# Performance work log

Hardware: AMD Instinct MI355X
Metric: run time of the kernel (lower is better)

Reference implementation:

```python
import jax, jax.numpy as jnp
import numpy as np

# static multi-scale feature pyramid (strides 8/16/32/64 of ~800px input)
SPATIAL = ((100, 100), (50, 50), (25, 25), (13, 13))
L = 4          # num_levels
NH = 8         # num_heads
NP = 4         # num_points
E = 256        # embed_dim
HD = E // NH   # head dim = 32
NLAYERS = 6
FFN_DIM = 1024
T = sum(h * w for h, w in SPATIAL)  # 13294 total tokens
B = 2


def _layer_norm(x, g, b, eps=1e-5):
    m = jnp.mean(x, -1, keepdims=True)
    v = jnp.mean((x - m) ** 2, -1, keepdims=True)
    return (x - m) * jax.lax.rsqrt(v + eps) * g + b


def _get_reference_points(valid_ratios):
    # valid_ratios: [B, L, 2] (wx, hy)
    refs = []
    for lvl, (H_, W_) in enumerate(SPATIAL):
        ry, rx = jnp.meshgrid(
            jnp.linspace(0.5, H_ - 0.5, H_, dtype=jnp.float32),
            jnp.linspace(0.5, W_ - 0.5, W_, dtype=jnp.float32),
            indexing='ij')
        ry = ry.reshape(-1)[None] / (valid_ratios[:, None, lvl, 1] * H_)
        rx = rx.reshape(-1)[None] / (valid_ratios[:, None, lvl, 0] * W_)
        refs.append(jnp.stack([rx, ry], -1))            # [B, H*W, 2]
    ref = jnp.concatenate(refs, 1)                       # [B, T, 2]
    return ref[:, :, None] * valid_ratios[:, None]       # [B, T, L, 2]


def _msda(value, loc, attn_w):
    # value: [B, T, NH, HD]; loc: [B, Q, NH, L, NP, 2] in [0,1]; attn_w: [B, Q, NH, L, NP]
    Bv, Tv, H, D = value.shape
    Q = loc.shape[1]
    out = jnp.zeros((Bv, Q, H, D), value.dtype)
    start = 0
    for lvl, (h, w) in enumerate(SPATIAL):
        v = value[:, start:start + h * w].transpose(0, 2, 1, 3)  # [B, NH, hw, D]
        start += h * w
        g = loc[:, :, :, lvl]                                    # [B, Q, NH, NP, 2]
        # grid_sample semantics, align_corners=False: pixel = g*size - 0.5
        x = g[..., 0] * w - 0.5
        y = g[..., 1] * h - 0.5
        x0 = jnp.floor(x).astype(jnp.int32)
        y0 = jnp.floor(y).astype(jnp.int32)
        wx = x - x0
        wy = y - y0

        def corner(ix, iy, cw):
            valid = (ix >= 0) & (ix < w) & (iy >= 0) & (iy < h)
            idx = jnp.clip(iy, 0, h - 1) * w + jnp.clip(ix, 0, w - 1)  # [B,Q,NH,NP]
            idx_t = idx.transpose(0, 2, 1, 3).reshape(Bv, H, Q * NP)
            gath = jnp.take_along_axis(v, idx_t[..., None], axis=2)    # [B,NH,QP,D]
            gath = gath.reshape(Bv, H, Q, NP, D)
            m = valid.transpose(0, 2, 1, 3)[..., None].astype(value.dtype)
            cw_t = cw.transpose(0, 2, 1, 3)[..., None]
            return gath * m * cw_t

        samp = (corner(x0, y0, (1 - wx) * (1 - wy))
                + corner(x0 + 1, y0, wx * (1 - wy))
                + corner(x0, y0 + 1, (1 - wx) * wy)
                + corner(x0 + 1, y0 + 1, wx * wy))  # [B,NH,Q,NP,D]
        out = out + jnp.einsum('bhqpd,bqhp->bqhd', samp, attn_w[:, :, :, lvl])
    return out.reshape(Bv, Q, H * D)


# offset normalizer (W, H) per level, as in Deformable-DETR
_OFF_NORM = jnp.array([[w, h] for (h, w) in SPATIAL], jnp.float32)  # [L, 2]


def _block(src, pos, ref, mask, p):
    (Wv, bv, Woff, boff, Wattn, battn, Wout, bout,
     n1g, n1b, n2g, n2b, W1, b1, W2, b2) = p
    x = _layer_norm(src, n1g, n1b)
    q = x + pos
    value = x @ Wv + bv
    value = jnp.where(mask[:, :, None], 0.0, value).reshape(B, T, NH, HD)
    off = (q @ Woff + boff).reshape(B, T, NH, L, NP, 2)
    attn = (q @ Wattn + battn).reshape(B, T, NH, L * NP)
    attn = jax.nn.softmax(attn, -1).reshape(B, T, NH, L, NP)
    loc = ref[:, :, None, :, None, :] + off / _OFF_NORM[None, None, None, :, None, :]
    attn_out = _msda(value, loc, attn) @ Wout + bout
    src = src + attn_out
    x = _layer_norm(src, n2g, n2b)
    ffn = jax.nn.relu(x @ W1 + b1) @ W2 + b2
    return src + ffn


def setup_inputs() -> dict:
    key = jax.random.key(0)
    ks = jax.random.split(key, 24)

    def rn(k, shape, scale=0.02):
        return jax.random.normal(k, shape, jnp.float32) * scale

    inp = {
        'src': jax.random.normal(ks[0], (B, T, E), jnp.float32),
        'pos': jax.random.normal(ks[1], (B, T, E), jnp.float32),
        'valid_ratios': jnp.ones((B, L, 2), jnp.float32),
        'spatial_shapes': jnp.array(SPATIAL, jnp.int32),
        'level_start_index': jnp.array(
            np.concatenate([[0], np.cumsum([h * w for h, w in SPATIAL])[:-1]]), jnp.int32),
        'mask': jnp.zeros((B, T), bool),
        # per-layer stacked parameters [NLAYERS, ...]
        'Wv': rn(ks[2], (NLAYERS, E, E)),
        'bv': jnp.zeros((NLAYERS, E), jnp.float32),
        'Woff': rn(ks[3], (NLAYERS, E, NH * L * NP * 2)),
        'boff': rn(ks[4], (NLAYERS, NH * L * NP * 2), 0.5),
        'Wattn': rn(ks[5], (NLAYERS, E, NH * L * NP)),
        'battn': jnp.zeros((NLAYERS, NH * L * NP), jnp.float32),
        'Wout': rn(ks[6], (NLAYERS, E, E)),
        'bout': jnp.zeros((NLAYERS, E), jnp.float32),
        'n1g': jnp.ones((NLAYERS, E), jnp.float32),
        'n1b': jnp.zeros((NLAYERS, E), jnp.float32),
        'n2g': jnp.ones((NLAYERS, E), jnp.float32),
        'n2b': jnp.zeros((NLAYERS, E), jnp.float32),
        'W1': rn(ks[7], (NLAYERS, E, FFN_DIM)),
        'b1': jnp.zeros((NLAYERS, FFN_DIM), jnp.float32),
        'W2': rn(ks[8], (NLAYERS, FFN_DIM, E)),
        'b2': jnp.zeros((NLAYERS, E), jnp.float32),
    }
    return inp


def reference(src, pos, valid_ratios, spatial_shapes, level_start_index, mask,
              Wv, bv, Woff, boff, Wattn, battn, Wout, bout,
              n1g, n1b, n2g, n2b, W1, b1, W2, b2):
    # spatial_shapes / level_start_index are encoded statically in SPATIAL (values match)
    ref = _get_reference_points(valid_ratios)  # [B, T, L, 2]
    x = src
    stacked = (Wv, bv, Woff, boff, Wattn, battn, Wout, bout,
               n1g, n1b, n2g, n2b, W1, b1, W2, b2)
    for i in range(NLAYERS):
        p = tuple(a[i] for a in stacked)
        x = _block(x, pos, ref, mask, p)
    return x
```

## Files before the change

### kernel.cpp

```cpp
#include <hip/hip_runtime.h>
#include <hip/hip_bf16.h>

#define NLAYERS 6
#define Bc 2
#define Tc 13294
#define Ec 256
#define NHc 8
#define FFNc 1024

#define EPI_BIAS 0
#define EPI_MASK 1
#define EPI_RES  2
#define EPI_RELU 3

typedef __attribute__((ext_vector_type(8))) short bf16x8;
typedef __attribute__((ext_vector_type(4))) float f32x4;

typedef __attribute__((address_space(3))) unsigned int u32_lds;
typedef __attribute__((address_space(1))) unsigned int u32_glb;

__device__ __forceinline__ void gld16(const void* g, void* l) {
    __builtin_amdgcn_global_load_lds((const u32_glb*)g, (u32_lds*)l, 16, 0, 0);
}

__device__ __forceinline__ short f2bf(float f) {
    union { float f; unsigned u; } v; v.f = f;
    unsigned r = v.u + 0x7FFFu + ((v.u >> 16) & 1u);
    return (short)(r >> 16);
}
__device__ __forceinline__ float bf2f(short s) {
    union { unsigned u; float f; } v; v.u = ((unsigned)(unsigned short)s) << 16;
    return v.f;
}
__device__ __forceinline__ float bf_lo(unsigned u) {
    union { unsigned u; float f; } v; v.u = u << 16; return v.f;
}
__device__ __forceinline__ float bf_hi(unsigned u) {
    union { unsigned u; float f; } v; v.u = u & 0xFFFF0000u; return v.f;
}

__global__ __launch_bounds__(256) void ln_kernel(
    const float* __restrict__ src, const float* __restrict__ pos,
    const float* __restrict__ g, const float* __restrict__ b,
    short* __restrict__ x, short* __restrict__ q, int rows)
{
    int wave = threadIdx.x >> 6;
    int lane = threadIdx.x & 63;
    int row = blockIdx.x * 4 + wave;
    if (row >= rows) return;
    const float* p = src + (size_t)row * Ec;
    float4 v = *(const float4*)(p + lane * 4);
    float s  = v.x + v.y + v.z + v.w;
    float sq = v.x*v.x + v.y*v.y + v.z*v.z + v.w*v.w;
    #pragma unroll
    for (int o = 32; o; o >>= 1) { s += __shfl_xor(s, o); sq += __shfl_xor(sq, o); }
    float mean = s * (1.f / Ec);
    float var  = sq * (1.f / Ec) - mean * mean;
    float inv  = rsqrtf(var + 1e-5f);
    float4 gg = *(const float4*)(g + lane * 4);
    float4 bb = *(const float4*)(b + lane * 4);
    float xo0 = (v.x - mean) * inv * gg.x + bb.x;
    float xo1 = (v.y - mean) * inv * gg.y + bb.y;
    float xo2 = (v.z - mean) * inv * gg.z + bb.z;
    float xo3 = (v.w - mean) * inv * gg.w + bb.w;
    short4 xs; xs.x = f2bf(xo0); xs.y = f2bf(xo1); xs.z = f2bf(xo2); xs.w = f2bf(xo3);
    *(short4*)(x + (size_t)row * Ec + lane * 4) = xs;
    if (q) {
        float4 pp = *(const float4*)(pos + (size_t)row * Ec + lane * 4);
        short4 qs;
        qs.x = f2bf(xo0 + pp.x); qs.y = f2bf(xo1 + pp.y);
        qs.z = f2bf(xo2 + pp.z); qs.w = f2bf(xo3 + pp.w);
        *(short4*)(q + (size_t)row * Ec + lane * 4) = qs;
    }
}

__global__ __launch_bounds__(256) void transpose_w(
    const float* __restrict__ W, short* __restrict__ Wt, int K, int N,
    int layerStride, int rowOff)
{
    __shared__ float tile[32][33];
    int l = blockIdx.z;
    const float* Wl = W + (size_t)l * K * N;
    short* Wtl = Wt + (size_t)l * layerStride;
    int n0 = blockIdx.x * 32, k0 = blockIdx.y * 32;
    int tx = threadIdx.x & 31, ty = threadIdx.x >> 5;
    #pragma unroll
    for (int i = 0; i < 32; i += 8)
        tile[ty + i][tx] = Wl[(size_t)(k0 + ty + i) * N + n0 + tx];
    __syncthreads();
    #pragma unroll
    for (int i = 0; i < 32; i += 8)
        Wtl[(size_t)(rowOff + n0 + ty + i) * K + k0 + tx] = f2bf(tile[tx][ty + i]);
}

template<int EPI, int OBF>
__global__ __launch_bounds__(256) void gemm_mfma(
    const short* __restrict__ A, const short* __restrict__ Bt,
    const float* __restrict__ bias, const float* __restrict__ bias2,
    const float* __restrict__ res, const unsigned char* __restrict__ mask,
    void* __restrict__ Cout, int M, int N, int K)
{
    __shared__ short As[2][128 * 32];
    __shared__ short Bs[2][64 * 32];
    const int tid = threadIdx.x;
    const int lane = tid & 63;
    const int wv = tid >> 6;
    const int row0 = blockIdx.x * 128;
    const int col0 = blockIdx.y * 64;
    const int mbase = (wv >> 1) * 64;
    const int nbase = (wv & 1) * 32;
    const int lr = lane & 15;
    const int kg = lane >> 4;

    f32x4 zf = {0.f, 0.f, 0.f, 0.f};
    f32x4 acc[4][2];
    #pragma unroll
    for (int i = 0; i < 4; ++i)
        #pragma unroll
        for (int j = 0; j < 2; ++j) acc[i][j] = zf;

    const int scol = (lane & 3) * 8;
    const int srowA = wv * 32 + (lane >> 2);
    const short* Ap = A + (size_t)(row0 + srowA) * K + scol;
    const int lA0 = srowA * 32 + scol;
    const int lA1 = lA0 + 16 * 32;
    const int srowB = wv * 16 + (lane >> 2);
    const short* Bp = Bt + (size_t)(col0 + srowB) * K + scol;
    const int lB = srowB * 32 + scol;

    #define STAGE(buf, k0) do { \
        gld16(Ap + (k0),                &As[buf][lA0]); \
        gld16(Ap + (size_t)16*K + (k0), &As[buf][lA1]); \
        gld16(Bp + (k0),                &Bs[buf][lB]); \
    } while (0)

    STAGE(0, 0);
    __syncthreads();
    int cur = 0;
    for (int k0 = 0; k0 < K; k0 += 32) {
        if (k0 + 32 < K) STAGE(cur ^ 1, k0 + 32);
        bf16x8 af[4], bfr[2];
        #pragma unroll
        for (int i = 0; i < 4; ++i)
            af[i]  = *(const bf16x8*)&As[cur][(mbase + i * 16 + lr) * 32 + kg * 8];
        #pragma unroll
        for (int j = 0; j < 2; ++j)
            bfr[j] = *(const bf16x8*)&Bs[cur][(nbase + j * 16 + lr) * 32 + kg * 8];
        #pragma unroll
        for (int mi = 0; mi < 4; ++mi)
            #pragma unroll
            for (int ni = 0; ni < 2; ++ni)
                acc[mi][ni] = __builtin_amdgcn_mfma_f32_16x16x32_bf16(
                    af[mi], bfr[ni], acc[mi][ni], 0, 0, 0);
        __syncthreads();
        cur ^= 1;
    }
    #undef STAGE

    float* Cf = (float*)Cout;
    short* Cb = (short*)Cout;
    #pragma unroll
    for (int ni = 0; ni < 2; ++ni) {
        int col = col0 + nbase + ni * 16 + lr;
        float bz = (bias2 && col >= 256) ? bias2[col - 256] : bias[col];
        #pragma unroll
        for (int mi = 0; mi < 4; ++mi) {
            int rb = row0 + mbase + mi * 16 + kg * 4;
            #pragma unroll
            for (int j = 0; j < 4; ++j) {
                int grow = rb + j;
                if (grow >= M) continue;
                float v = acc[mi][ni][j] + bz;
                if (EPI == EPI_MASK) { if (mask[grow]) v = 0.f; }
                if (EPI == EPI_RES)  v += res[(size_t)grow * N + col];
                if (EPI == EPI_RELU) v = v > 0.f ? v : 0.f;
                if (OBF) Cb[(size_t)grow * N + col] = f2bf(v);
                else     Cf[(size_t)grow * N + col] = v;
            }
        }
    }
}

__global__ __launch_bounds__(256) void msda_kernel(
    const short* __restrict__ value, const short* __restrict__ oa,
    const float* __restrict__ vr, short* __restrict__ out)
{
    __shared__ int pts[8 * 136];
    const int group = threadIdx.x >> 5;
    const int l32 = threadIdx.x & 31;
    const int gidx = blockIdx.x * 8 + group;
    const int h = gidx & 7;
    const int bq = gidx >> 3;
    const int b = (bq >= Tc) ? 1 : 0;
    const int qq = bq - b * Tc;

    if (l32 < 16) {
        const int p = l32;
        const int lvl = p >> 2;
        const int Wl[4] = {100, 50, 25, 13};
        const int St[4] = {0, 10000, 12500, 13125};
        float base_x, base_y;
        if (qq < 10000) {
            int qi = qq;
            base_x = (0.5f + (float)(qi % 100)) / (vr[(b*4+0)*2+0] * 100.f);
            base_y = (0.5f + (float)(qi / 100)) / (vr[(b*4+0)*2+1] * 100.f);
        } else if (qq < 12500) {
            int qi = qq - 10000;
            base_x = (0.5f + (float)(qi % 50)) / (vr[(b*4+1)*2+0] * 50.f);
            base_y = (0.5f + (float)(qi / 50)) / (vr[(b*4+1)*2+1] * 50.f);
        } else if (qq < 13125) {
            int qi = qq - 12500;
            base_x = (0.5f + (float)(qi % 25)) / (vr[(b*4+2)*2+0] * 25.f);
            base_y = (0.5f + (float)(qi / 25)) / (vr[(b*4+2)*2+1] * 25.f);
        } else {
            int qi = qq - 13125;
            base_x = (0.5f + (float)(qi % 13)) / (vr[(b*4+3)*2+0] * 13.f);
            base_y = (0.5f + (float)(qi / 13)) / (vr[(b*4+3)*2+1] * 13.f);
        }
        float logit = bf2f(oa[(size_t)bq * 384 + 256 + h * 16 + p]);
        float mx = logit;
        #pragma unroll
        for (int o = 8; o; o >>= 1) mx = fmaxf(mx, __shfl_xor(mx, o));
        float e = expf(logit - mx);
        float sum = e;
        #pragma unroll
        for (int o = 8; o; o >>= 1) sum += __shfl_xor(sum, o);
        float aw = e / sum;

        const int w = Wl[lvl], hh = Wl[lvl];
        const float refx = base_x * vr[(b*4+lvl)*2+0];
        const float refy = base_y * vr[(b*4+lvl)*2+1];
        const float ox = bf2f(oa[(size_t)bq * 384 + h * 32 + p * 2 + 0]);
        const float oy = bf2f(oa[(size_t)bq * 384 + h * 32 + p * 2 + 1]);
        float locx = refx + ox / (float)w;
        float locy = refy + oy / (float)hh;
        float xf = locx * (float)w - 0.5f;
        float yf = locy * (float)hh - 0.5f;
        float x0f = floorf(xf), y0f = floorf(yf);
        int x0 = (int)x0f, y0 = (int)y0f;
        float wx = xf - x0f, wy = yf - y0f;
        float w00 = (1.f - wx) * (1.f - wy) * aw;
        float w10 = wx * (1.f - wy) * aw;
        float w01 = (1.f - wx) * wy * aw;
        float w11 = wx * wy * aw;
        bool vx0 = (x0 >= 0) && (x0 < w);
        bool vx1 = (x0 + 1 >= 0) && (x0 + 1 < w);
        bool vy0 = (y0 >= 0) && (y0 < hh);
        bool vy1 = (y0 + 1 >= 0) && (y0 + 1 < hh);
        if (!(vx0 && vy0)) w00 = 0.f;
        if (!(vx1 && vy0)) w10 = 0.f;
        if (!(vx0 && vy1)) w01 = 0.f;
        if (!(vx1 && vy1)) w11 = 0.f;
        int cx0 = min(max(x0, 0), w - 1), cx1 = min(max(x0 + 1, 0), w - 1);
        int cy0 = min(max(y0, 0), hh - 1), cy1 = min(max(y0 + 1, 0), hh - 1);
        int rowbase = b * Tc + St[lvl];
        int slot = group * 136 + p * 8 + ((p >> 3) & 1) * 4;
        int4 wq4; wq4.x = __float_as_int(w00); wq4.y = __float_as_int(w10);
        wq4.z = __float_as_int(w01); wq4.w = __float_as_int(w11);
        int4 aq4;
        aq4.x = (rowbase + cy0 * w + cx0) * 512 + h * 64;
        aq4.y = (rowbase + cy0 * w + cx1) * 512 + h * 64;
        aq4.z = (rowbase + cy1 * w + cx0) * 512 + h * 64;
        aq4.w = (rowbase + cy1 * w + cx1) * 512 + h * 64;
        *(int4*)&pts[slot] = wq4;
        *(int4*)&pts[slot + 4] = aq4;
    }
    __syncthreads();

    const int d4 = (l32 & 15) * 4;
    const int ph = (l32 >> 4) * 8;
    const int xw = (l32 >> 4) * 4;
    const char* vbase = (const char*)value;
    float accL = 0.f, accH = 0.f;
    #pragma unroll
    for (int j = 0; j < 8; ++j) {
        int p = ph + j;
        int slot = group * 136 + p * 8 + xw;
        int4 wq = *(const int4*)&pts[slot];
        int4 aq = *(const int4*)&pts[slot + 4];
        unsigned u0 = *(const unsigned*)(vbase + (unsigned)(aq.x + d4));
        unsigned u1 = *(const unsigned*)(vbase + (unsigned)(aq.y + d4));
        unsigned u2 = *(const unsigned*)(vbase + (unsigned)(aq.z + d4));
        unsigned u3 = *(const unsigned*)(vbase + (unsigned)(aq.w + d4));
        float w00 = __int_as_float(wq.x), w10 = __int_as_float(wq.y);
        float w01 = __int_as_float(wq.z), w11 = __int_as_float(wq.w);
        accL = fmaf(w00, bf_lo(u0), accL); accH = fmaf(w00, bf_hi(u0), accH);
        accL = fmaf(w10, bf_lo(u1), accL); accH = fmaf(w10, bf_hi(u1), accH);
        accL = fmaf(w01, bf_lo(u2), accL); accH = fmaf(w01, bf_hi(u2), accH);
        accL = fmaf(w11, bf_lo(u3), accL); accH = fmaf(w11, bf_hi(u3), accH);
    }
    accL += __shfl_xor(accL, 16);
    accH += __shfl_xor(accH, 16);
    if (l32 < 16) {
        unsigned pk = ((unsigned)(unsigned short)f2bf(accL)) |
                      (((unsigned)(unsigned short)f2bf(accH)) << 16);
        *(unsigned*)((char*)out + (size_t)bq * 512 + h * 64 + d4) = pk;
    }
}

extern "C" void kernel_launch(void* const* d_in, const int* in_sizes, int n_in,
                              void* d_out, int out_size, void* d_ws, size_t ws_size,
                              hipStream_t stream) {
    const float* src  = (const float*)d_in[0];
    const float* pos  = (const float*)d_in[1];
    const float* vr   = (const float*)d_in[2];
    const unsigned char* mask = (const unsigned char*)d_in[5];
    const float* Wv    = (const float*)d_in[6];
    const float* bv    = (const float*)d_in[7];
    const float* Woff  = (const float*)d_in[8];
    const float* boff  = (const float*)d_in[9];
    const float* Wattn = (const float*)d_in[10];
    const float* battn = (const float*)d_in[11];
    const float* Wout  = (const float*)d_in[12];
    const float* bout  = (const float*)d_in[13];
    const float* n1g   = (const float*)d_in[14];
    const float* n1b   = (const float*)d_in[15];
    const float* n2g   = (const float*)d_in[16];
    const float* n2b   = (const float*)d_in[17];
    const float* W1    = (const float*)d_in[18];
    const float* b1    = (const float*)d_in[19];
    const float* W2    = (const float*)d_in[20];
    const float* b2    = (const float*)d_in[21];
    float* out = (float*)d_out;

    const size_t R = (size_t)Bc * Tc;

    short* xb    = (short*)d_ws;
    short* qb    = xb + R * 256;
    short* valb  = qb + R * 256;
    short* msdab = valb + R * 256;
    short* oab   = msdab + R * 256;
    short* ln2b  = xb;
    short* hb    = qb;
    float* srcb  = (float*)(oab + R * 384);
    short* wvT   = (short*)(srcb + R * 256);
    short* woaT  = wvT + 6 * 65536;
    short* woutT = woaT + 6 * 98304;
    short* w1T   = woutT + 6 * 65536;
    short* w2T   = w1T + 6 * 262144;

    transpose_w<<<dim3(8, 8, 6),  256, 0, stream>>>(Wv,    wvT,   256, 256,  65536, 0);
    transpose_w<<<dim3(8, 8, 6),  256, 0, stream>>>(Woff,  woaT,  256, 256,  98304, 0);
    transpose_w<<<dim3(4, 8, 6),  256, 0, stream>>>(Wattn, woaT,  256, 128,  98304, 256);
    transpose_w<<<dim3(8, 8, 6),  256, 0, stream>>>(Wout,  woutT, 256, 256,  65536, 0);
    transpose_w<<<dim3(32, 8, 6), 256, 0, stream>>>(W1,    w1T,   256, 1024, 262144, 0);
    transpose_w<<<dim3(8, 32, 6), 256, 0, stream>>>(W2,    w2T,   1024, 256, 262144, 0);

    const int lnBlocks = (int)((R + 3) / 4);
    const int MT = (int)((R + 127) / 128);

    for (int l = 0; l < NLAYERS; ++l) {
        const float* cur = (l == 0) ? src : srcb;
        ln_kernel<<<lnBlocks, 256, 0, stream>>>(cur, pos, n1g + l * Ec, n1b + l * Ec, xb, qb, (int)R);
        gemm_mfma<EPI_MASK, 1><<<dim3(MT, 4), 256, 0, stream>>>(
            xb, wvT + (size_t)l * 65536, bv + l * Ec, nullptr, nullptr, mask, valb, (int)R, 256, 256);
        gemm_mfma<EPI_BIAS, 1><<<dim3(MT, 6), 256, 0, stream>>>(
            qb, woaT + (size_t)l * 98304, boff + l * 256, battn + l * 128, nullptr, nullptr,
            oab, (int)R, 384, 256);
        msda_kernel<<<(int)R, 256, 0, stream>>>(valb, oab, vr, msdab);
        gemm_mfma<EPI_RES, 0><<<dim3(MT, 4), 256, 0, stream>>>(
            msdab, woutT + (size_t)l * 65536, bout + l * Ec, nullptr, cur, nullptr, srcb, (int)R, 256, 256);
        ln_kernel<<<lnBlocks, 256, 0, stream>>>(srcb, nullptr, n2g + l * Ec, n2b + l * Ec, ln2b, nullptr, (int)R);
        gemm_mfma<EPI_RELU, 1><<<dim3(MT, 16), 256, 0, stream>>>(
            ln2b, w1T + (size_t)l * 262144, b1 + l * FFNc, nullptr, nullptr, nullptr, hb, (int)R, 1024, 256);
        float* dst = (l == NLAYERS - 1) ? out : srcb;
        gemm_mfma<EPI_RES, 0><<<dim3(MT, 4), 256, 0, stream>>>(
            hb, w2T + (size_t)l * 262144, b2 + l * Ec, nullptr, srcb, nullptr, dst, (int)R, 256, 1024);
    }
}
```

Baseline: 1.250 ms.

## Fuse LayerNorm into full-row GEMM epilogues and enlarge FFN/offset GEMM tiles

Adds a full-row (64x256) GEMM kernel whose epilogue computes LayerNorm across the four waves through LDS. It is used for the output projection (producing norm2) and the FFN down projection (producing the next layer's norm1 and the query-plus-pos buffer), which removes the separate LN launches and their extra fp32 read of the activations. The offset/attention and FFN up-projection GEMMs move to 128x128 tiles, and the MSDA bf16 high-half extraction drops its mask. The risks are less parallelism per launch for the full-row GEMM (about 416 blocks), higher register pressure, and a new workspace layout where hb aliases valb.

```diff
diff --git a/kernel.cpp b/kernel.cpp
--- a/kernel.cpp
+++ b/kernel.cpp
@@ -34,9 +34,6 @@
 }
 __device__ __forceinline__ float bf_lo(unsigned u) {
     union { unsigned u; float f; } v; v.u = u << 16; return v.f;
-}
-__device__ __forceinline__ float bf_hi(unsigned u) {
-    union { unsigned u; float f; } v; v.u = u & 0xFFFF0000u; return v.f;
 }
 
 __global__ __launch_bounds__(256) void ln_kernel(
@@ -65,13 +62,11 @@
     float xo3 = (v.w - mean) * inv * gg.w + bb.w;
     short4 xs; xs.x = f2bf(xo0); xs.y = f2bf(xo1); xs.z = f2bf(xo2); xs.w = f2bf(xo3);
     *(short4*)(x + (size_t)row * Ec + lane * 4) = xs;
-    if (q) {
-        float4 pp = *(const float4*)(pos + (size_t)row * Ec + lane * 4);
-        short4 qs;
-        qs.x = f2bf(xo0 + pp.x); qs.y = f2bf(xo1 + pp.y);
-        qs.z = f2bf(xo2 + pp.z); qs.w = f2bf(xo3 + pp.w);
-        *(short4*)(q + (size_t)row * Ec + lane * 4) = qs;
-    }
+    float4 pp = *(const float4*)(pos + (size_t)row * Ec + lane * 4);
+    short4 qs;
+    qs.x = f2bf(xo0 + pp.x); qs.y = f2bf(xo1 + pp.y);
+    qs.z = f2bf(xo2 + pp.z); qs.w = f2bf(xo3 + pp.w);
+    *(short4*)(q + (size_t)row * Ec + lane * 4) = qs;
 }
 
 __global__ __launch_bounds__(256) void transpose_w(
@@ -93,45 +88,50 @@
         Wtl[(size_t)(rowOff + n0 + ty + i) * K + k0 + tx] = f2bf(tile[tx][ty + i]);
 }
 
-template<int EPI, int OBF>
-__global__ __launch_bounds__(256) void gemm_mfma(
+template<int EPI, int OBF, int WLN, int WQ>
+__global__ __launch_bounds__(256) void gemm_row(
     const short* __restrict__ A, const short* __restrict__ Bt,
-    const float* __restrict__ bias, const float* __restrict__ bias2,
-    const float* __restrict__ res, const unsigned char* __restrict__ mask,
-    void* __restrict__ Cout, int M, int N, int K)
+    const float* __restrict__ bias, const float* __restrict__ res,
+    const unsigned char* __restrict__ mask, void* __restrict__ sout,
+    const float* __restrict__ g, const float* __restrict__ b,
+    short* __restrict__ lnout, short* __restrict__ qout,
+    const float* __restrict__ pos, int M, int K)
 {
-    __shared__ short As[2][128 * 32];
-    __shared__ short Bs[2][64 * 32];
+    __shared__ short As[2][64 * 32];
+    __shared__ short Bs[2][256 * 32];
+    __shared__ float lnred[64][4][2];
     const int tid = threadIdx.x;
     const int lane = tid & 63;
     const int wv = tid >> 6;
-    const int row0 = blockIdx.x * 128;
-    const int col0 = blockIdx.y * 64;
-    const int mbase = (wv >> 1) * 64;
-    const int nbase = (wv & 1) * 32;
+    const int row0 = blockIdx.x * 64;
     const int lr = lane & 15;
     const int kg = lane >> 4;
 
     f32x4 zf = {0.f, 0.f, 0.f, 0.f};
-    f32x4 acc[4][2];
+    f32x4 acc[4][4];
     #pragma unroll
     for (int i = 0; i < 4; ++i)
         #pragma unroll
-        for (int j = 0; j < 2; ++j) acc[i][j] = zf;
+        for (int j = 0; j < 4; ++j) acc[i][j] = zf;
 
     const int scol = (lane & 3) * 8;
-    const int srowA = wv * 32 + (lane >> 2);
-    const short* Ap = A + (size_t)(row0 + srowA) * K + scol;
-    const int lA0 = srowA * 32 + scol;
-    const int lA1 = lA0 + 16 * 32;
-    const int srowB = wv * 16 + (lane >> 2);
-    const short* Bp = Bt + (size_t)(col0 + srowB) * K + scol;
-    const int lB = srowB * 32 + scol;
+    const int sr = wv * 16 + (lane >> 2);
+    const short* Ap = A + (size_t)(row0 + sr) * K + scol;
+    const int lA = sr * 32 + scol;
+    const short* Bp[4];
+    int lB[4];
+    #pragma unroll
+    for (int i = 0; i < 4; ++i) {
+        Bp[i] = Bt + (size_t)(i * 64 + sr) * K + scol;
+        lB[i] = (i * 64 + sr) * 32 + scol;
+    }
 
     #define STAGE(buf, k0) do { \
-        gld16(Ap + (k0),                &As[buf][lA0]); \
-        gld16(Ap + (size_t)16*K + (k0), &As[buf][lA1]); \
-        gld16(Bp + (k0),                &Bs[buf][lB]); \
+        gld16(Ap + (k0), &As[buf][lA]); \
+        gld16(Bp[0] + (k0), &Bs[buf][lB[0]]); \
+        gld16(Bp[1] + (k0), &Bs[buf][lB[1]]); \
+        gld16(Bp[2] + (k0), &Bs[buf][lB[2]]); \
+        gld16(Bp[3] + (k0), &Bs[buf][lB[3]]); \
     } while (0)
 
     STAGE(0, 0);
@@ -139,17 +139,16 @@
     int cur = 0;
     for (int k0 = 0; k0 < K; k0 += 32) {
         if (k0 + 32 < K) STAGE(cur ^ 1, k0 + 32);
-        bf16x8 af[4], bfr[2];
-        #pragma unroll
-        for (int i = 0; i < 4; ++i)
-            af[i]  = *(const bf16x8*)&As[cur][(mbase + i * 16 + lr) * 32 + kg * 8];
-        #pragma unroll
-        for (int j = 0; j < 2; ++j)
-            bfr[j] = *(const bf16x8*)&Bs[cur][(nbase + j * 16 + lr) * 32 + kg * 8];
+        bf16x8 af[4], bfr[4];
+        #pragma unroll
+        for (int i = 0; i < 4; ++i) {
+            af[i]  = *(const bf16x8*)&As[cur][(i * 16 + lr) * 32 + kg * 8];
+            bfr[i] = *(const bf16x8*)&Bs[cur][(wv * 64 + i * 16 + lr) * 32 + kg * 8];
+        }
         #pragma unroll
         for (int mi = 0; mi < 4; ++mi)
             #pragma unroll
-            for (int ni = 0; ni < 2; ++ni)
+            for (int ni = 0; ni < 4; ++ni)
                 acc[mi][ni] = __builtin_amdgcn_mfma_f32_16x16x32_bf16(
                     af[mi], bfr[ni], acc[mi][ni], 0, 0, 0);
         __syncthreads();
@@ -157,10 +156,162 @@
     }
     #undef STAGE
 
-    float* Cf = (float*)Cout;
-    short* Cb = (short*)Cout;
-    #pragma unroll
-    for (int ni = 0; ni < 2; ++ni) {
+    float* Sf = (float*)sout;
+    short* Sb = (short*)sout;
+    float bz[4];
+    #pragma unroll
+    for (int ni = 0; ni < 4; ++ni) bz[ni] = bias[wv * 64 + ni * 16 + lr];
+    #pragma unroll
+    for (int mi = 0; mi < 4; ++mi) {
+        #pragma unroll
+        for (int j = 0; j < 4; ++j) {
+            int grow = row0 + mi * 16 + kg * 4 + j;
+            bool ok = grow < M;
+            bool mz = (EPI == EPI_MASK) && ok && mask[grow];
+            #pragma unroll
+            for (int ni = 0; ni < 4; ++ni) {
+                int col = wv * 64 + ni * 16 + lr;
+                float v = acc[mi][ni][j] + bz[ni];
+                if (EPI == EPI_RES && ok) v += res[(size_t)grow * 256 + col];
+                if (EPI == EPI_MASK && mz) v = 0.f;
+                acc[mi][ni][j] = v;
+                if (ok) {
+                    if (OBF) Sb[(size_t)grow * 256 + col] = f2bf(v);
+                    else     Sf[(size_t)grow * 256 + col] = v;
+                }
+            }
+        }
+    }
+
+    if (WLN) {
+        float s[16], sq[16];
+        #pragma unroll
+        for (int mi = 0; mi < 4; ++mi)
+            #pragma unroll
+            for (int j = 0; j < 4; ++j) {
+                float ss = 0.f, qq = 0.f;
+                #pragma unroll
+                for (int ni = 0; ni < 4; ++ni) {
+                    float v = acc[mi][ni][j];
+                    ss += v; qq += v * v;
+                }
+                s[mi * 4 + j] = ss; sq[mi * 4 + j] = qq;
+            }
+        #pragma unroll
+        for (int o = 1; o < 16; o <<= 1) {
+            #pragma unroll
+            for (int idx = 0; idx < 16; ++idx) {
+                s[idx]  += __shfl_xor(s[idx], o);
+                sq[idx] += __shfl_xor(sq[idx], o);
+            }
+        }
+        if (lr == 0) {
+            #pragma unroll
+            for (int mi = 0; mi < 4; ++mi)
+                #pragma unroll
+                for (int j = 0; j < 4; ++j) {
+                    int r = mi * 16 + kg * 4 + j;
+                    lnred[r][wv][0] = s[mi * 4 + j];
+                    lnred[r][wv][1] = sq[mi * 4 + j];
+                }
+        }
+        __syncthreads();
+        float gg[4], bb[4];
+        #pragma unroll
+        for (int ni = 0; ni < 4; ++ni) {
+            int col = wv * 64 + ni * 16 + lr;
+            gg[ni] = g[col]; bb[ni] = b[col];
+        }
+        #pragma unroll
+        for (int mi = 0; mi < 4; ++mi) {
+            #pragma unroll
+            for (int j = 0; j < 4; ++j) {
+                int r = mi * 16 + kg * 4 + j;
+                int grow = row0 + r;
+                float S = lnred[r][0][0] + lnred[r][1][0] + lnred[r][2][0] + lnred[r][3][0];
+                float Q = lnred[r][0][1] + lnred[r][1][1] + lnred[r][2][1] + lnred[r][3][1];
+                float mean = S * (1.f / 256.f);
+                float var  = Q * (1.f / 256.f) - mean * mean;
+                float inv  = rsqrtf(var + 1e-5f);
+                bool ok = grow < M;
+                #pragma unroll
+                for (int ni = 0; ni < 4; ++ni) {
+                    int col = wv * 64 + ni * 16 + lr;
+                    float o = (acc[mi][ni][j] - mean) * inv * gg[ni] + bb[ni];
+                    if (ok) {
+                        lnout[(size_t)grow * 256 + col] = f2bf(o);
+                        if (WQ) qout[(size_t)grow * 256 + col] =
+                            f2bf(o + pos[(size_t)grow * 256 + col]);
+                    }
+                }
+            }
+        }
+    }
+}
+
+template<int EPI>
+__global__ __launch_bounds__(256) void gemm128(
+    const short* __restrict__ A, const short* __restrict__ Bt,
+    const float* __restrict__ bias, const float* __restrict__ bias2,
+    short* __restrict__ Cout, int M, int N, int K)
+{
+    __shared__ short As[2][128 * 32];
+    __shared__ short Bs[2][128 * 32];
+    const int tid = threadIdx.x;
+    const int lane = tid & 63;
+    const int wv = tid >> 6;
+    const int row0 = blockIdx.x * 128;
+    const int col0 = blockIdx.y * 128;
+    const int mbase = (wv >> 1) * 64;
+    const int nbase = (wv & 1) * 64;
+    const int lr = lane & 15;
+    const int kg = lane >> 4;
+
+    f32x4 zf = {0.f, 0.f, 0.f, 0.f};
+    f32x4 acc[4][4];
+    #pragma unroll
+    for (int i = 0; i < 4; ++i)
+        #pragma unroll
+        for (int j = 0; j < 4; ++j) acc[i][j] = zf;
+
+    const int scol = (lane & 3) * 8;
+    const int sr = wv * 32 + (lane >> 2);
+    const short* Ap = A + (size_t)(row0 + sr) * K + scol;
+    const short* Bp = Bt + (size_t)(col0 + sr) * K + scol;
+    const int l0 = sr * 32 + scol;
+    const int l1 = l0 + 16 * 32;
+
+    #define STAGE(buf, k0) do { \
+        gld16(Ap + (k0),                &As[buf][l0]); \
+        gld16(Ap + (size_t)16*K + (k0), &As[buf][l1]); \
+        gld16(Bp + (k0),                &Bs[buf][l0]); \
+        gld16(Bp + (size_t)16*K + (k0), &Bs[buf][l1]); \
+    } while (0)
+
+    STAGE(0, 0);
+    __syncthreads();
+    int cur = 0;
+    for (int k0 = 0; k0 < K; k0 += 32) {
+        if (k0 + 32 < K) STAGE(cur ^ 1, k0 + 32);
+        bf16x8 af[4], bfr[4];
+        #pragma unroll
+        for (int i = 0; i < 4; ++i) {
+            af[i]  = *(const bf16x8*)&As[cur][(mbase + i * 16 + lr) * 32 + kg * 8];
+            bfr[i] = *(const bf16x8*)&Bs[cur][(nbase + i * 16 + lr) * 32 + kg * 8];
+        }
+        #pragma unroll
+        for (int mi = 0; mi < 4; ++mi)
+            #pragma unroll
+            for (int ni = 0; ni < 4; ++ni)
+                acc[mi][ni] = __builtin_amdgcn_mfma_f32_16x16x32_bf16(
+                    af[mi], bfr[ni], acc[mi][ni], 0, 0, 0);
+        __syncthreads();
+        cur ^= 1;
+    }
+    #undef STAGE
+
+    #pragma unroll
+    for (int ni = 0; ni < 4; ++ni) {
         int col = col0 + nbase + ni * 16 + lr;
         float bz = (bias2 && col >= 256) ? bias2[col - 256] : bias[col];
         #pragma unroll
@@ -171,11 +322,8 @@
                 int grow = rb + j;
                 if (grow >= M) continue;
                 float v = acc[mi][ni][j] + bz;
-                if (EPI == EPI_MASK) { if (mask[grow]) v = 0.f; }
-                if (EPI == EPI_RES)  v += res[(size_t)grow * N + col];
                 if (EPI == EPI_RELU) v = v > 0.f ? v : 0.f;
-                if (OBF) Cb[(size_t)grow * N + col] = f2bf(v);
-                else     Cf[(size_t)grow * N + col] = v;
+                Cout[(size_t)grow * N + col] = f2bf(v);
             }
         }
     }
@@ -284,10 +432,10 @@
         unsigned u3 = *(const unsigned*)(vbase + (unsigned)(aq.w + d4));
         float w00 = __int_as_float(wq.x), w10 = __int_as_float(wq.y);
         float w01 = __int_as_float(wq.z), w11 = __int_as_float(wq.w);
-        accL = fmaf(w00, bf_lo(u0), accL); accH = fmaf(w00, bf_hi(u0), accH);
-        accL = fmaf(w10, bf_lo(u1), accL); accH = fmaf(w10, bf_hi(u1), accH);
-        accL = fmaf(w01, bf_lo(u2), accL); accH = fmaf(w01, bf_hi(u2), accH);
-        accL = fmaf(w11, bf_lo(u3), accL); accH = fmaf(w11, bf_hi(u3), accH);
+        accL = fmaf(w00, bf_lo(u0), accL); accH = fmaf(w00, __int_as_float((int)u0), accH);
+        accL = fmaf(w10, bf_lo(u1), accL); accH = fmaf(w10, __int_as_float((int)u1), accH);
+        accL = fmaf(w01, bf_lo(u2), accL); accH = fmaf(w01, __int_as_float((int)u2), accH);
+        accL = fmaf(w11, bf_lo(u3), accL); accH = fmaf(w11, __int_as_float((int)u3), accH);
     }
     accL += __shfl_xor(accL, 16);
     accH += __shfl_xor(accH, 16);
@@ -331,8 +479,8 @@
     short* msdab = valb + R * 256;
     short* oab   = msdab + R * 256;
     short* ln2b  = xb;
-    short* hb    = qb;
-    float* srcb  = (float*)(oab + R * 384);
+    short* hb    = valb;
+    float* srcb  = (float*)(oab + R * 384 + R * 128);
     short* wvT   = (short*)(srcb + R * 256);
     short* woaT  = wvT + 6 * 65536;
     short* woutT = woaT + 6 * 98304;
@@ -346,25 +494,33 @@
     transpose_w<<<dim3(32, 8, 6), 256, 0, stream>>>(W1,    w1T,   256, 1024, 262144, 0);
     transpose_w<<<dim3(8, 32, 6), 256, 0, stream>>>(W2,    w2T,   1024, 256, 262144, 0);
 
-    const int lnBlocks = (int)((R + 3) / 4);
-    const int MT = (int)((R + 127) / 128);
+    const int M = (int)R;
+    const int RT = (int)((R + 63) / 64);
+    const int MT2 = (int)((R + 127) / 128);
+
+    ln_kernel<<<(int)((R + 3) / 4), 256, 0, stream>>>(src, pos, n1g, n1b, xb, qb, M);
 
     for (int l = 0; l < NLAYERS; ++l) {
         const float* cur = (l == 0) ? src : srcb;
-        ln_kernel<<<lnBlocks, 256, 0, stream>>>(cur, pos, n1g + l * Ec, n1b + l * Ec, xb, qb, (int)R);
-        gemm_mfma<EPI_MASK, 1><<<dim3(MT, 4), 256, 0, stream>>>(
-            xb, wvT + (size_t)l * 65536, bv + l * Ec, nullptr, nullptr, mask, valb, (int)R, 256, 256);
-        gemm_mfma<EPI_BIAS, 1><<<dim3(MT, 6), 256, 0, stream>>>(
-            qb, woaT + (size_t)l * 98304, boff + l * 256, battn + l * 128, nullptr, nullptr,
-            oab, (int)R, 384, 256);
+        gemm_row<EPI_MASK, 1, 0, 0><<<RT, 256, 0, stream>>>(
+            xb, wvT + (size_t)l * 65536, bv + l * Ec, nullptr, mask, valb,
+            nullptr, nullptr, nullptr, nullptr, nullptr, M, 256);
+        gemm128<EPI_BIAS><<<dim3(MT2, 3), 256, 0, stream>>>(
+            qb, woaT + (size_t)l * 98304, boff + l * 256, battn + l * 128, oab, M, 384, 256);
         msda_kernel<<<(int)R, 256, 0, stream>>>(valb, oab, vr, msdab);
-        gemm_mfma<EPI_RES, 0><<<dim3(MT, 4), 256, 0, stream>>>(
-            msdab, woutT + (size_t)l * 65536, bout + l * Ec, nullptr, cur, nullptr, srcb, (int)R, 256, 256);
-        ln_kernel<<<lnBlocks, 256, 0, stream>>>(srcb, nullptr, n2g + l * Ec, n2b + l * Ec, ln2b, nullptr, (int)R);
-        gemm_mfma<EPI_RELU, 1><<<dim3(MT, 16), 256, 0, stream>>>(
-            ln2b, w1T + (size_t)l * 262144, b1 + l * FFNc, nullptr, nullptr, nullptr, hb, (int)R, 1024, 256);
-        float* dst = (l == NLAYERS - 1) ? out : srcb;
-        gemm_mfma<EPI_RES, 0><<<dim3(MT, 4), 256, 0, stream>>>(
-            hb, w2T + (size_t)l * 262144, b2 + l * Ec, nullptr, srcb, nullptr, dst, (int)R, 256, 1024);
-    }
-}
+        gemm_row<EPI_RES, 0, 1, 0><<<RT, 256, 0, stream>>>(
+            msdab, woutT + (size_t)l * 65536, bout + l * Ec, cur, nullptr, srcb,
+            n2g + l * Ec, n2b + l * Ec, ln2b, nullptr, nullptr, M, 256);
+        gemm128<EPI_RELU><<<dim3(MT2, 8), 256, 0, stream>>>(
+            ln2b, w1T + (size_t)l * 262144, b1 + l * FFNc, nullptr, hb, M, 1024, 256);
+        if (l < NLAYERS - 1) {
+            gemm_row<EPI_RES, 0, 1, 1><<<RT, 256, 0, stream>>>(
+                hb, w2T + (size_t)l * 262144, b2 + l * Ec, srcb, nullptr, srcb,
+                n1g + (l + 1) * Ec, n1b + (l + 1) * Ec, xb, qb, pos, M, 1024);
+        } else {
+            gemm_row<EPI_RES, 0, 0, 0><<<RT, 256, 0, stream>>>(
+                hb, w2T + (size_t)l * 262144, b2 + l * Ec, srcb, nullptr, out,
+                nullptr, nullptr, nullptr, nullptr, nullptr, M, 1024);
+        }
+    }
+}
```

New measurement: 1.345 ms. 7.6% more time.

## Store residual stream and positional embeddings in bf16 between layers

Applied to the files above, without the earlier changes.

Keeps the residual activation buffer in bf16 instead of fp32, adds a bf16 layer norm kernel, and pre-converts the positional embedding to bf16 once. The GEMM epilogues read the residual in bf16 and write bf16, so every layer moves less memory through the residual and layer-norm path. The MSDA inner loop also drops a mask when extracting the high bf16 half. This adds bf16 rounding error that accumulates in the residual across six layers.

```diff
diff --git a/kernel.cpp b/kernel.cpp
--- a/kernel.cpp
+++ b/kernel.cpp
@@ -35,8 +35,15 @@
 __device__ __forceinline__ float bf_lo(unsigned u) {
     union { unsigned u; float f; } v; v.u = u << 16; return v.f;
 }
-__device__ __forceinline__ float bf_hi(unsigned u) {
-    union { unsigned u; float f; } v; v.u = u & 0xFFFF0000u; return v.f;
+
+__global__ __launch_bounds__(256) void f2bf_kernel(
+    const float* __restrict__ in, short* __restrict__ out, int n4)
+{
+    int i = blockIdx.x * 256 + threadIdx.x;
+    if (i >= n4) return;
+    float4 v = *(const float4*)(in + (size_t)i * 4);
+    short4 s; s.x = f2bf(v.x); s.y = f2bf(v.y); s.z = f2bf(v.z); s.w = f2bf(v.w);
+    *(short4*)(out + (size_t)i * 4) = s;
 }
 
 __global__ __launch_bounds__(256) void ln_kernel(
@@ -65,11 +72,44 @@
     float xo3 = (v.w - mean) * inv * gg.w + bb.w;
     short4 xs; xs.x = f2bf(xo0); xs.y = f2bf(xo1); xs.z = f2bf(xo2); xs.w = f2bf(xo3);
     *(short4*)(x + (size_t)row * Ec + lane * 4) = xs;
+    float4 pp = *(const float4*)(pos + (size_t)row * Ec + lane * 4);
+    short4 qs;
+    qs.x = f2bf(xo0 + pp.x); qs.y = f2bf(xo1 + pp.y);
+    qs.z = f2bf(xo2 + pp.z); qs.w = f2bf(xo3 + pp.w);
+    *(short4*)(q + (size_t)row * Ec + lane * 4) = qs;
+}
+
+__global__ __launch_bounds__(256) void ln_bf_kernel(
+    const short* __restrict__ src, const short* __restrict__ pos,
+    const float* __restrict__ g, const float* __restrict__ b,
+    short* __restrict__ x, short* __restrict__ q, int rows)
+{
+    int wave = threadIdx.x >> 6;
+    int lane = threadIdx.x & 63;
+    int row = blockIdx.x * 4 + wave;
+    if (row >= rows) return;
+    short4 v4 = *(const short4*)(src + (size_t)row * Ec + lane * 4);
+    float v0 = bf2f(v4.x), v1 = bf2f(v4.y), v2 = bf2f(v4.z), v3 = bf2f(v4.w);
+    float s  = v0 + v1 + v2 + v3;
+    float sq = v0*v0 + v1*v1 + v2*v2 + v3*v3;
+    #pragma unroll
+    for (int o = 32; o; o >>= 1) { s += __shfl_xor(s, o); sq += __shfl_xor(sq, o); }
+    float mean = s * (1.f / Ec);
+    float var  = sq * (1.f / Ec) - mean * mean;
+    float inv  = rsqrtf(var + 1e-5f);
+    float4 gg = *(const float4*)(g + lane * 4);
+    float4 bb = *(const float4*)(b + lane * 4);
+    float xo0 = (v0 - mean) * inv * gg.x + bb.x;
+    float xo1 = (v1 - mean) * inv * gg.y + bb.y;
+    float xo2 = (v2 - mean) * inv * gg.z + bb.z;
+    float xo3 = (v3 - mean) * inv * gg.w + bb.w;
+    short4 xs; xs.x = f2bf(xo0); xs.y = f2bf(xo1); xs.z = f2bf(xo2); xs.w = f2bf(xo3);
+    *(short4*)(x + (size_t)row * Ec + lane * 4) = xs;
     if (q) {
-        float4 pp = *(const float4*)(pos + (size_t)row * Ec + lane * 4);
+        short4 pp = *(const short4*)(pos + (size_t)row * Ec + lane * 4);
         short4 qs;
-        qs.x = f2bf(xo0 + pp.x); qs.y = f2bf(xo1 + pp.y);
-        qs.z = f2bf(xo2 + pp.z); qs.w = f2bf(xo3 + pp.w);
+        qs.x = f2bf(xo0 + bf2f(pp.x)); qs.y = f2bf(xo1 + bf2f(pp.y));
+        qs.z = f2bf(xo2 + bf2f(pp.z)); qs.w = f2bf(xo3 + bf2f(pp.w));
         *(short4*)(q + (size_t)row * Ec + lane * 4) = qs;
     }
 }
@@ -93,11 +133,12 @@
         Wtl[(size_t)(rowOff + n0 + ty + i) * K + k0 + tx] = f2bf(tile[tx][ty + i]);
 }
 
-template<int EPI, int OBF>
+template<int EPI, int OBF, int RESBF>
 __global__ __launch_bounds__(256) void gemm_mfma(
     const short* __restrict__ A, const short* __restrict__ Bt,
     const float* __restrict__ bias, const float* __restrict__ bias2,
-    const float* __restrict__ res, const unsigned char* __restrict__ mask,
+    const float* __restrict__ resf, const short* __restrict__ resb,
+    const unsigned char* __restrict__ mask,
     void* __restrict__ Cout, int M, int N, int K)
 {
     __shared__ short As[2][128 * 32];
@@ -172,7 +213,10 @@
                 if (grow >= M) continue;
                 float v = acc[mi][ni][j] + bz;
                 if (EPI == EPI_MASK) { if (mask[grow]) v = 0.f; }
-                if (EPI == EPI_RES)  v += res[(size_t)grow * N + col];
+                if (EPI == EPI_RES) {
+                    v += RESBF ? bf2f(resb[(size_t)grow * N + col])
+                               : resf[(size_t)grow * N + col];
+                }
                 if (EPI == EPI_RELU) v = v > 0.f ? v : 0.f;
                 if (OBF) Cb[(size_t)grow * N + col] = f2bf(v);
                 else     Cf[(size_t)grow * N + col] = v;
@@ -284,10 +328,10 @@
         unsigned u3 = *(const unsigned*)(vbase + (unsigned)(aq.w + d4));
         float w00 = __int_as_float(wq.x), w10 = __int_as_float(wq.y);
         float w01 = __int_as_float(wq.z), w11 = __int_as_float(wq.w);
-        accL = fmaf(w00, bf_lo(u0), accL); accH = fmaf(w00, bf_hi(u0), accH);
-        accL = fmaf(w10, bf_lo(u1), accL); accH = fmaf(w10, bf_hi(u1), accH);
-        accL = fmaf(w01, bf_lo(u2), accL); accH = fmaf(w01, bf_hi(u2), accH);
-        accL = fmaf(w11, bf_lo(u3), accL); accH = fmaf(w11, bf_hi(u3), accH);
+        accL = fmaf(w00, bf_lo(u0), accL); accH = fmaf(w00, __int_as_float((int)u0), accH);
+        accL = fmaf(w10, bf_lo(u1), accL); accH = fmaf(w10, __int_as_float((int)u1), accH);
+        accL = fmaf(w01, bf_lo(u2), accL); accH = fmaf(w01, __int_as_float((int)u2), accH);
+        accL = fmaf(w11, bf_lo(u3), accL); accH = fmaf(w11, __int_as_float((int)u3), accH);
     }
     accL += __shfl_xor(accL, 16);
     accH += __shfl_xor(accH, 16);
@@ -330,10 +374,11 @@
     short* valb  = qb + R * 256;
     short* msdab = valb + R * 256;
     short* oab   = msdab + R * 256;
+    short* srcb  = oab + R * 384;
+    short* posb  = srcb + R * 256;
     short* ln2b  = xb;
     short* hb    = qb;
-    float* srcb  = (float*)(oab + R * 384);
-    short* wvT   = (short*)(srcb + R * 256);
+    short* wvT   = posb + R * 256;
     short* woaT  = wvT + 6 * 65536;
     short* woutT = woaT + 6 * 98304;
     short* w1T   = woutT + 6 * 65536;
@@ -345,26 +390,45 @@
     transpose_w<<<dim3(8, 8, 6),  256, 0, stream>>>(Wout,  woutT, 256, 256,  65536, 0);
     transpose_w<<<dim3(32, 8, 6), 256, 0, stream>>>(W1,    w1T,   256, 1024, 262144, 0);
     transpose_w<<<dim3(8, 32, 6), 256, 0, stream>>>(W2,    w2T,   1024, 256, 262144, 0);
-
+    f2bf_kernel<<<(int)((R * 64 + 255) / 256), 256, 0, stream>>>(pos, posb, (int)(R * 64));
+
+    const int M = (int)R;
     const int lnBlocks = (int)((R + 3) / 4);
     const int MT = (int)((R + 127) / 128);
 
+    ln_kernel<<<lnBlocks, 256, 0, stream>>>(src, pos, n1g, n1b, xb, qb, M);
+
     for (int l = 0; l < NLAYERS; ++l) {
-        const float* cur = (l == 0) ? src : srcb;
-        ln_kernel<<<lnBlocks, 256, 0, stream>>>(cur, pos, n1g + l * Ec, n1b + l * Ec, xb, qb, (int)R);
-        gemm_mfma<EPI_MASK, 1><<<dim3(MT, 4), 256, 0, stream>>>(
-            xb, wvT + (size_t)l * 65536, bv + l * Ec, nullptr, nullptr, mask, valb, (int)R, 256, 256);
-        gemm_mfma<EPI_BIAS, 1><<<dim3(MT, 6), 256, 0, stream>>>(
+        gemm_mfma<EPI_MASK, 1, 0><<<dim3(MT, 4), 256, 0, stream>>>(
+            xb, wvT + (size_t)l * 65536, bv + l * Ec, nullptr, nullptr, nullptr, mask,
+            valb, M, 256, 256);
+        gemm_mfma<EPI_BIAS, 1, 0><<<dim3(MT, 6), 256, 0, stream>>>(
             qb, woaT + (size_t)l * 98304, boff + l * 256, battn + l * 128, nullptr, nullptr,
-            oab, (int)R, 384, 256);
+            nullptr, oab, M, 384, 256);
         msda_kernel<<<(int)R, 256, 0, stream>>>(valb, oab, vr, msdab);
-        gemm_mfma<EPI_RES, 0><<<dim3(MT, 4), 256, 0, stream>>>(
-            msdab, woutT + (size_t)l * 65536, bout + l * Ec, nullptr, cur, nullptr, srcb, (int)R, 256, 256);
-        ln_kernel<<<lnBlocks, 256, 0, stream>>>(srcb, nullptr, n2g + l * Ec, n2b + l * Ec, ln2b, nullptr, (int)R);
-        gemm_mfma<EPI_RELU, 1><<<dim3(MT, 16), 256, 0, stream>>>(
-            ln2b, w1T + (size_t)l * 262144, b1 + l * FFNc, nullptr, nullptr, nullptr, hb, (int)R, 1024, 256);
-        float* dst = (l == NLAYERS - 1) ? out : srcb;
-        gemm_mfma<EPI_RES, 0><<<dim3(MT, 4), 256, 0, stream>>>(
-            hb, w2T + (size_t)l * 262144, b2 + l * Ec, nullptr, srcb, nullptr, dst, (int)R, 256, 1024);
-    }
-}
+        if (l == 0)
+            gemm_mfma<EPI_RES, 1, 0><<<dim3(MT, 4), 256, 0, stream>>>(
+                msdab, woutT + (size_t)l * 65536, bout + l * Ec, nullptr, src, nullptr,
+                nullptr, srcb, M, 256, 256);
+        else
+            gemm_mfma<EPI_RES, 1, 1><<<dim3(MT, 4), 256, 0, stream>>>(
+                msdab, woutT + (size_t)l * 65536, bout + l * Ec, nullptr, nullptr, srcb,
+                nullptr, srcb, M, 256, 256);
+        ln_bf_kernel<<<lnBlocks, 256, 0, stream>>>(srcb, nullptr, n2g + l * Ec, n2b + l * Ec,
+                                                   ln2b, nullptr, M);
+        gemm_mfma<EPI_RELU, 1, 0><<<dim3(MT, 16), 256, 0, stream>>>(
+            ln2b, w1T + (size_t)l * 262144, b1 + l * FFNc, nullptr, nullptr, nullptr, nullptr,
+            hb, M, 1024, 256);
+        if (l < NLAYERS - 1) {
+            gemm_mfma<EPI_RES, 1, 1><<<dim3(MT, 4), 256, 0, stream>>>(
+                hb, w2T + (size_t)l * 262144, b2 + l * Ec, nullptr, nullptr, srcb,
+                nullptr, srcb, M, 256, 1024);
+            ln_bf_kernel<<<lnBlocks, 256, 0, stream>>>(srcb, posb, n1g + (l + 1) * Ec,
+                                                       n1b + (l + 1) * Ec, xb, qb, M);
+        } else {
+            gemm_mfma<EPI_RES, 0, 1><<<dim3(MT, 4), 256, 0, stream>>>(
+                hb, w2T + (size_t)l * 262144, b2 + l * Ec, nullptr, nullptr, srcb,
+                nullptr, out, M, 256, 1024);
+        }
+    }
+}
```

Measured after the change: 1.181 ms. 1.06x faster.
